# Kernel optimization log

Measured on AMD Instinct MI355X. Metric: run time of the kernel, lower is better.

## Reference

```python
import jax, jax.numpy as jnp
import numpy as np


def setup_inputs() -> dict:
    key = jax.random.key(0)
    kx, ks = jax.random.split(key)
    X = jax.random.normal(kx, (8, 4096, 16), dtype=jnp.float32)
    # nn.Parameter(torch.rand(1) + 1.0)
    sigma = jax.random.uniform(ks, (1,), dtype=jnp.float32) + 1.0
    return {"X": X, "sigma": sigma}


def reference(X, sigma):
    sq = jnp.sum(X * X, axis=-1)                       # [B, N]
    inner = jnp.einsum('bnf,bmf->bnm', X, X)           # [B, N, N]
    sqdist = sq[:, :, None] + sq[:, None, :] - 2.0 * inner
    sqdist = jnp.maximum(sqdist, 0.0)                  # guard tiny negatives
    gaussian = jnp.exp(-sqdist / sigma[0])             # [B, N, N]
    # original _softmax: exp(gaussian) / sum over dim 2 == softmax over axis 2
    return jax.nn.softmax(gaussian, axis=2)
```

## Files before the change

### kernel.cpp

```cpp
#include <hip/hip_runtime.h>


typedef float v4f __attribute__((ext_vector_type(4)));
typedef short bf8 __attribute__((ext_vector_type(8)));

constexpr int Bn  = 8;
constexpr int N   = 4096;
constexpr int F   = 16;
constexpr int BM  = 16;
constexpr int BLK = 1024;
constexpr int NW  = BLK / 64;
constexpr int TPW = (N / 16) / NW;

__device__ __forceinline__ unsigned short f2bf(float x) {
    unsigned int u = __float_as_uint(x);
    unsigned int r = (u + 0x7FFFu + ((u >> 16) & 1u)) >> 16;
    return (unsigned short)r;
}
__device__ __forceinline__ float bf2f(unsigned short h) {
    return __uint_as_float(((unsigned int)h) << 16);
}
__device__ __forceinline__ float uni(float x) {
    return __int_as_float(__builtin_amdgcn_readfirstlane(__float_as_int(x)));
}

__global__ __launch_bounds__(256)
void pack_kernel(const float* __restrict__ X, uint4* __restrict__ Xp,
                 float* __restrict__ sqm) {
    const int b = blockIdx.y;
    const int m = blockIdx.x * 256 + threadIdx.x;
    const float4* src = (const float4*)(X + ((size_t)b * N + m) * F);
    const float4 v0 = src[0], v1 = src[1], v2 = src[2], v3 = src[3];
    const float x[F] = {v0.x, v0.y, v0.z, v0.w, v1.x, v1.y, v1.z, v1.w,
                        v2.x, v2.y, v2.z, v2.w, v3.x, v3.y, v3.z, v3.w};
    float s = 0.f;
    #pragma unroll
    for (int f = 0; f < F; ++f) s = fmaf(x[f], x[f], s);
    sqm[(size_t)b * N + m] = s;

    uint4* dst = Xp + ((size_t)b * N + m) * 4;
    #pragma unroll
    for (int g = 0; g < 4; ++g) {
        unsigned int hi[4], lo[4];
        #pragma unroll
        for (int j = 0; j < 4; ++j) {
            const float xf = x[4 * g + j];
            const unsigned short h = f2bf(xf);
            hi[j] = h;
            lo[j] = f2bf(xf - bf2f(h));
        }
        uint4 c;
        c.x = hi[0] | (hi[1] << 16);
        c.y = hi[2] | (hi[3] << 16);
        c.z = lo[0] | (lo[1] << 16);
        c.w = lo[2] | (lo[3] << 16);
        dst[g] = c;
    }
}

union BfU { uint4 u; bf8 h; };

__global__ __launch_bounds__(BLK)
void gs_mfma(const uint4* __restrict__ Xp, const float* __restrict__ sqm,
             const float* __restrict__ sigma_p, float* __restrict__ out) {
    __shared__ float red[NW][BM];

    const int tid  = threadIdx.x;
    const int w    = tid >> 6;
    const int lane = tid & 63;
    const int g    = lane >> 4;
    const int c    = lane & 15;
    const int b    = blockIdx.y;
    const int n0   = blockIdx.x * BM;

    const uint4* Xpb = Xp + (size_t)b * N * 4;
    const float* sqb = sqm + (size_t)b * N;

    BfU b1; b1.u = Xpb[(size_t)(n0 + c) * 4 + g];
    BfU b2; b2.u = make_uint4(b1.u.z, b1.u.w, b1.u.x, b1.u.y);

    const float sqn_l = sqb[n0 + c];
    const float nis   = uni(-1.0f / sigma_p[0]);

    v4f e[TPW];
    float psum = 0.f;

    #pragma unroll
    for (int t = 0; t < TPW; ++t) {
        const int m_tile = w * (TPW * 16) + t * 16;
        BfU a; a.u = Xpb[(size_t)(m_tile + c) * 4 + g];

        v4f acc = {0.f, 0.f, 0.f, 0.f};
        acc = __builtin_amdgcn_mfma_f32_16x16x32_bf16(a.h, b1.h, acc, 0, 0, 0);
        acc = __builtin_amdgcn_mfma_f32_16x16x32_bf16(a.h, b2.h, acc, 0, 0, 0);

        const v4f sm4 = *(const v4f*)(sqb + m_tile + 4 * g);
        v4f ev;
        ev.x = __expf(__expf(fmaxf(fmaf(-2.f, acc.x, sqn_l + sm4.x), 0.f) * nis));
        ev.y = __expf(__expf(fmaxf(fmaf(-2.f, acc.y, sqn_l + sm4.y), 0.f) * nis));
        ev.z = __expf(__expf(fmaxf(fmaf(-2.f, acc.z, sqn_l + sm4.z), 0.f) * nis));
        ev.w = __expf(__expf(fmaxf(fmaf(-2.f, acc.w, sqn_l + sm4.w), 0.f) * nis));
        e[t] = ev;
        psum += (ev.x + ev.y) + (ev.z + ev.w);
    }

    psum += __shfl_xor(psum, 16, 64);
    psum += __shfl_xor(psum, 32, 64);
    if (lane < 16) red[w][lane] = psum;
    __syncthreads();

    float tot = 0.f;
    #pragma unroll
    for (int w2 = 0; w2 < NW; ++w2) tot += red[w2][c];
    const float inv = 1.0f / tot;

    float* rowp = out + ((size_t)b * N + n0 + c) * (size_t)N;
    #pragma unroll
    for (int t = 0; t < TPW; ++t) {
        const int m_tile = w * (TPW * 16) + t * 16;
        v4f v = e[t] * inv;
        __builtin_nontemporal_store(v, (v4f*)(rowp + m_tile + 4 * g));
    }
}

extern "C" void kernel_launch(void* const* d_in, const int* in_sizes, int n_in,
                              void* d_out, int out_size, void* d_ws, size_t ws_size,
                              hipStream_t stream) {
    const float* X     = (const float*)d_in[0];
    const float* sigma = (const float*)d_in[1];
    float* out         = (float*)d_out;
    uint4* Xp          = (uint4*)d_ws;
    float* sqm         = (float*)d_ws + (size_t)Bn * N * 16;

    pack_kernel<<<dim3(N / 256, Bn), 256, 0, stream>>>(X, Xp, sqm);
    gs_mfma<<<dim3(N / BM, Bn), BLK, 0, stream>>>(Xp, sqm, sigma, out);
}
```

Before: 607.3 us.

## Stage softmax numerators in LDS as bf16 and store full rows per wave

Instead of holding the exponentials in registers and writing scattered 16-byte chunks across 16 rows, each wave now writes bf16-packed values into a swizzled LDS buffer. After the reduction, each wave reads back a whole row and writes it contiguously. The aim is to make global stores fully coalesced and to cut register pressure. In exchange it rounds the numerators to bf16, which lowers output precision, and it uses about 128KB of dynamic LDS per block.

```diff
diff --git a/kernel.cpp b/kernel.cpp
--- a/kernel.cpp
+++ b/kernel.cpp
@@ -63,7 +63,9 @@
 __global__ __launch_bounds__(BLK)
 void gs_mfma(const uint4* __restrict__ Xp, const float* __restrict__ sqm,
              const float* __restrict__ sigma_p, float* __restrict__ out) {
-    __shared__ float red[NW][BM];
+    extern __shared__ char smem[];
+    unsigned short (*lds_e)[N] = (unsigned short (*)[N])smem;
+    float* red = (float*)(smem + (size_t)BM * N * 2);
 
     const int tid  = threadIdx.x;
     const int w    = tid >> 6;
@@ -82,7 +84,6 @@
     const float sqn_l = sqb[n0 + c];
     const float nis   = uni(-1.0f / sigma_p[0]);
 
-    v4f e[TPW];
     float psum = 0.f;
 
     #pragma unroll
@@ -95,31 +96,42 @@
         acc = __builtin_amdgcn_mfma_f32_16x16x32_bf16(a.h, b2.h, acc, 0, 0, 0);
 
         const v4f sm4 = *(const v4f*)(sqb + m_tile + 4 * g);
-        v4f ev;
-        ev.x = __expf(__expf(fmaxf(fmaf(-2.f, acc.x, sqn_l + sm4.x), 0.f) * nis));
-        ev.y = __expf(__expf(fmaxf(fmaf(-2.f, acc.y, sqn_l + sm4.y), 0.f) * nis));
-        ev.z = __expf(__expf(fmaxf(fmaf(-2.f, acc.z, sqn_l + sm4.z), 0.f) * nis));
-        ev.w = __expf(__expf(fmaxf(fmaf(-2.f, acc.w, sqn_l + sm4.w), 0.f) * nis));
-        e[t] = ev;
-        psum += (ev.x + ev.y) + (ev.z + ev.w);
+        float ex = __expf(__expf(fmaxf(fmaf(-2.f, acc.x, sqn_l + sm4.x), 0.f) * nis));
+        float ey = __expf(__expf(fmaxf(fmaf(-2.f, acc.y, sqn_l + sm4.y), 0.f) * nis));
+        float ez = __expf(__expf(fmaxf(fmaf(-2.f, acc.z, sqn_l + sm4.z), 0.f) * nis));
+        float ew = __expf(__expf(fmaxf(fmaf(-2.f, acc.w, sqn_l + sm4.w), 0.f) * nis));
+
+        ushort4 pk;
+        pk.x = f2bf(ex); pk.y = f2bf(ey); pk.z = f2bf(ez); pk.w = f2bf(ew);
+        const int gl = (m_tile >> 2) + g;
+        const int gp = gl ^ (c << 2);
+        *(ushort4*)&lds_e[c][4 * gp] = pk;
+
+        psum += (ex + ey) + (ez + ew);
     }
 
     psum += __shfl_xor(psum, 16, 64);
     psum += __shfl_xor(psum, 32, 64);
-    if (lane < 16) red[w][lane] = psum;
+    if (lane < 16) red[w * BM + lane] = psum;
     __syncthreads();
 
     float tot = 0.f;
     #pragma unroll
-    for (int w2 = 0; w2 < NW; ++w2) tot += red[w2][c];
-    const float inv = 1.0f / tot;
+    for (int w2 = 0; w2 < NW; ++w2) tot += red[w2 * BM + w];
+    const float inv = uni(1.0f / tot);
 
-    float* rowp = out + ((size_t)b * N + n0 + c) * (size_t)N;
+    float* rowp = out + ((size_t)b * N + n0 + w) * (size_t)N;
     #pragma unroll
-    for (int t = 0; t < TPW; ++t) {
-        const int m_tile = w * (TPW * 16) + t * 16;
-        v4f v = e[t] * inv;
-        __builtin_nontemporal_store(v, (v4f*)(rowp + m_tile + 4 * g));
+    for (int k = 0; k < N / 4 / 64; ++k) {
+        const int gp = 64 * k + lane;
+        const int gl = gp ^ (w << 2);
+        const ushort4 pk = *(const ushort4*)&lds_e[w][4 * gp];
+        v4f v;
+        v.x = bf2f(pk.x) * inv;
+        v.y = bf2f(pk.y) * inv;
+        v.z = bf2f(pk.z) * inv;
+        v.w = bf2f(pk.w) * inv;
+        __builtin_nontemporal_store(v, (v4f*)rowp + gl);
     }
 }
 
@@ -132,6 +144,7 @@
     uint4* Xp          = (uint4*)d_ws;
     float* sqm         = (float*)d_ws + (size_t)Bn * N * 16;
 
+    const size_t lds_bytes = (size_t)BM * N * 2 + NW * BM * 4;
     pack_kernel<<<dim3(N / 256, Bn), 256, 0, stream>>>(X, Xp, sqm);
-    gs_mfma<<<dim3(N / BM, Bn), BLK, 0, stream>>>(Xp, sqm, sigma, out);
+    gs_mfma<<<dim3(N / BM, Bn), BLK, lds_bytes, stream>>>(Xp, sqm, sigma, out);
 }
```

After: 555.6 us. 1.09x faster.
